# Kernel tuning notes

Measured on AMD Instinct MI355X. Metric: run time of the kernel, lower is better.

## Reference

```python
import jax, jax.numpy as jnp
import numpy as np


def setup_inputs() -> dict:
    key = jax.random.key(0)
    kq, kk, kv = jax.random.split(key, 3)
    B, T, D = 32, 2048, 64
    return {
        "queries": jax.random.normal(kq, (B, T, D), dtype=jnp.float32),
        "keys": jax.random.normal(kk, (B, T, D), dtype=jnp.float32),
        "values": jax.random.normal(kv, (B, T, D), dtype=jnp.float32),
    }


def reference(queries, keys, values):
    # scores: [B, T, T] = Q K^T / sqrt(d)
    d = queries.shape[-1]
    scale = 1.0 / jnp.sqrt(jnp.asarray(d, dtype=queries.dtype))
    scores = jnp.einsum("btd,bsd->bts", queries, keys) * scale
    T = scores.shape[-1]
    # causal lower-triangular mask; masked positions -> -inf before softmax
    causal = jnp.tril(jnp.ones((T, T), dtype=bool))
    scores = jnp.where(causal[None, :, :], scores, -jnp.inf)
    attn = jax.nn.softmax(scores, axis=-1)
    # eval mode: no dropout
    return jnp.einsum("bts,bsd->btd", attn, values)
```

## Files before the change

### kernel.cpp

```cpp
#include <hip/hip_runtime.h>
#include <hip/hip_bf16.h>

typedef __bf16 bf16;
typedef bf16 bf16x2 __attribute__((ext_vector_type(2)));
typedef bf16 bf16x8 __attribute__((ext_vector_type(8)));
typedef float f32x2 __attribute__((ext_vector_type(2)));
typedef float f32x4 __attribute__((ext_vector_type(4)));
typedef float f32x16 __attribute__((ext_vector_type(16)));
typedef unsigned int uint;

namespace {
constexpr int kB  = 32;
constexpr int kT  = 2048;
constexpr int kD  = 64;
constexpr int QB  = 128;
constexpr float THR = 8.f;
constexpr int CHUNK_F = 128 * 64 + 128 + 128;
constexpr size_t WS_NEED = (size_t)512 * CHUNK_F * 4;
}

__global__ __launch_bounds__(256, 2)
void fa_part(const float* __restrict__ Qg, const float* __restrict__ Kg,
             const float* __restrict__ Vg, float* __restrict__ Og,
             float* __restrict__ Wg, int mode) {
  const int tid  = (int)threadIdx.x;
  const int wid  = tid >> 6;
  const int lane = tid & 63;
  const int hi   = lane >> 5;
  const int ql   = lane & 31;

  const int bid = (int)blockIdx.x;
  const int b   = bid & 31;
  const int u   = bid >> 5;
  int j, t0, t1, sc = 0; bool split;
  if (mode) {
    static const signed char JT[24] = {15,15,7,14,14,13,13,6,12,12,11,11,5,10,10,9,9,4,8,8,3,2,1,0};
    static const signed char HT[24] = { 0, 1,-1, 0, 1, 0, 1,-1, 0, 1, 0, 1,-1, 0, 1, 0, 1,-1, 0, 1,-1,-1,-1,-1};
    j = JT[u]; const int h = HT[u];
    if (h < 0) { split = false; t0 = 0; t1 = 2 * (j + 1); }
    else { split = true; t0 = h * (j + 1); t1 = t0 + (j + 1); sc = b * 16 + 2 * (15 - j) + h; }
  } else {
    j = 15 - u; split = false; t0 = 0; t1 = 2 * (j + 1);
  }
  const int q0   = j * QB;
  const int qw   = q0 + wid * 32;
  const int qrow = qw + ql;

  __shared__ __align__(16) char smem[4 * 32 * 36 * 4];
  bf16* lK = (bf16*)smem;
  bf16* lV = (bf16*)(smem + 8192);

  const float* Qb = Qg + ((size_t)b * kT + qw) * kD;
  const float* Kb = Kg + (size_t)b * kT * kD;
  const float* Vb = Vg + (size_t)b * kT * kD;
  float*       Ob = Og + ((size_t)b * kT + qw) * kD;

  bf16x8 qf[4];
#pragma unroll
  for (int db = 0; db < 4; ++db) {
    const float* s = Qb + (size_t)ql * kD + db * 16 + hi * 8;
    f32x4 f0 = *(const f32x4*)s, f1 = *(const f32x4*)(s + 4);
    bf16x8 q;
#pragma unroll
    for (int jj = 0; jj < 4; ++jj) {
      q[jj]     = (bf16)(f0[jj] * 0.125f);
      q[jj + 4] = (bf16)(f1[jj] * 0.125f);
    }
    qf[db] = q;
  }

  f32x16 ot0 = {}, ot1 = {};
  float m_s = -1e30f, l_s = 0.f;

  const int krow = tid >> 2;
  const int kc16 = (tid & 3) << 4;
  const int vkey = (tid & 31) << 1;
  const int vd0  = (tid >> 5) << 3;

  f32x4 kp0, kp1, kp2, kp3, vp0, vp1, vp2, vp3;

#define LOADK(KV)                                                      \
  {                                                                    \
    const float* s_ = Kb + (size_t)((KV) + krow) * kD + kc16;          \
    kp0 = ((const f32x4*)s_)[0]; kp1 = ((const f32x4*)s_)[1];          \
    kp2 = ((const f32x4*)s_)[2]; kp3 = ((const f32x4*)s_)[3];          \
  }
#define LOADV(KV)                                                      \
  {                                                                    \
    const float* s0_ = Vb + (size_t)((KV) + vkey) * kD + vd0;          \
    const float* s1_ = s0_ + kD;                                       \
    vp0 = ((const f32x4*)s0_)[0]; vp1 = ((const f32x4*)s0_)[1];        \
    vp2 = ((const f32x4*)s1_)[0]; vp3 = ((const f32x4*)s1_)[1];        \
  }
#define STAGEK()                                                       \
  {                                                                    \
    bf16x8 h0_, h1_;                                                   \
    _Pragma("unroll") for (int jj = 0; jj < 4; ++jj) {                 \
      h0_[jj] = (bf16)kp0[jj]; h0_[jj + 4] = (bf16)kp1[jj];            \
      h1_[jj] = (bf16)kp2[jj]; h1_[jj + 4] = (bf16)kp3[jj];            \
    }                                                                  \
    *(bf16x8*)&lK[(krow * 64 + kc16)     ^ ((krow & 7) << 3)] = h0_;   \
    *(bf16x8*)&lK[(krow * 64 + kc16 + 8) ^ ((krow & 7) << 3)] = h1_;   \
  }
#define STAGEV()                                                       \
  {                                                                    \
    _Pragma("unroll") for (int jj = 0; jj < 8; ++jj) {                 \
      int d_ = vd0 + jj;                                               \
      float a0_ = (jj < 4) ? vp0[jj] : vp1[jj - 4];                    \
      float a1_ = (jj < 4) ? vp2[jj] : vp3[jj - 4];                    \
      int e_ = (d_ * 64 + vkey) ^ ((d_ & 7) << 3);                     \
      *(bf16x2*)&lV[e_] = (bf16x2){(bf16)a0_, (bf16)a1_};              \
    }                                                                  \
  }

  const int kv0 = t0 * 64, kv1 = t1 * 64;
  LOADK(kv0) LOADV(kv0)
  for (int kv = kv0; kv < kv1; kv += 64) {
    STAGEK() STAGEV()
    __syncthreads();
    if (kv + 64 < kv1) { LOADK(kv + 64) LOADV(kv + 64) }

    if (kv <= qw) {
      const int nkb = (kv + 32 <= qw) ? 2 : 1;

      f32x16 st0 = {}, st1 = {};
      __builtin_amdgcn_s_setprio(1);
#pragma unroll
      for (int db = 0; db < 4; ++db) {
        bf16x8 kf = *(const bf16x8*)&lK[(ql * 64 + db * 16 + hi * 8) ^ ((ql & 7) << 3)];
        st0 = __builtin_amdgcn_mfma_f32_32x32x16_bf16(kf, qf[db], st0, 0, 0, 0);
      }
      if (nkb == 2) {
        const int r1 = 32 + ql;
#pragma unroll
        for (int db = 0; db < 4; ++db) {
          bf16x8 kf = *(const bf16x8*)&lK[(r1 * 64 + db * 16 + hi * 8) ^ ((r1 & 7) << 3)];
          st1 = __builtin_amdgcn_mfma_f32_32x32x16_bf16(kf, qf[db], st1, 0, 0, 0);
        }
      }
      __builtin_amdgcn_s_setprio(0);

      if (kv + (nkb << 5) > qw) {
#pragma unroll
        for (int reg = 0; reg < 16; ++reg) {
          int krel = (reg & 3) + 8 * (reg >> 2) + 4 * hi;
          if (kv + krel > qrow) st0[reg] = -1e30f;
          if (nkb == 2 && kv + 32 + krel > qrow) st1[reg] = -1e30f;
        }
      }

      float mx = -1e30f;
#pragma unroll
      for (int r = 0; r < 16; ++r) mx = fmaxf(mx, st0[r]);
      if (nkb == 2) {
#pragma unroll
        for (int r = 0; r < 16; ++r) mx = fmaxf(mx, st1[r]);
      }
      mx = fmaxf(mx, __shfl_xor(mx, 32));
      const bool defer = (__all((mx - m_s) <= THR) != 0);
      float mn = m_s;
      if (!defer) {
        mn = fmaxf(m_s, mx);
        float corr = __expf(m_s - mn);
        m_s = mn;
        l_s *= corr;
#pragma unroll
        for (int r = 0; r < 16; ++r) { ot0[r] *= corr; ot1[r] *= corr; }
      }
      float ls = 0.f;
#pragma unroll
      for (int r = 0; r < 16; ++r) { float p = __expf(st0[r] - mn); st0[r] = p; ls += p; }
      if (nkb == 2) {
#pragma unroll
        for (int r = 0; r < 16; ++r) { float p = __expf(st1[r] - mn); st1[r] = p; ls += p; }
      }
      ls += __shfl_xor(ls, 32);
      l_s += ls;

      uint w_[16];
#pragma unroll
      for (int m = 0; m < 8; ++m) {
        bf16x2 t = {(bf16)st0[2 * m], (bf16)st0[2 * m + 1]};
        w_[m] = __builtin_bit_cast(uint, t);
      }
      if (nkb == 2) {
#pragma unroll
        for (int m = 0; m < 8; ++m) {
          bf16x2 t = {(bf16)st1[2 * m], (bf16)st1[2 * m + 1]};
          w_[8 + m] = __builtin_bit_cast(uint, t);
        }
      }

#pragma unroll
      for (int ks = 0; ks < 4; ++ks) {
        if (ks < 2 * nkb) {
          const int mb = (ks >> 1) * 8 + (ks & 1) * 4;
          uint a0 = w_[mb], a1 = w_[mb + 1], b0 = w_[mb + 2], b1 = w_[mb + 3];
          asm volatile("v_permlane32_swap_b32 %0, %1" : "+v"(a0), "+v"(b0));
          asm volatile("v_permlane32_swap_b32 %0, %1" : "+v"(a1), "+v"(b1));
          union { uint u4[4]; bf16x8 v; } pc;
          pc.u4[0] = a0; pc.u4[1] = a1; pc.u4[2] = b0; pc.u4[3] = b1;
          const bf16x8 pf = pc.v;
          __builtin_amdgcn_s_setprio(1);
          {
            bf16x8 vf0 = *(const bf16x8*)&lV[(ql * 64 + ks * 16 + hi * 8) ^ ((ql & 7) << 3)];
            ot0 = __builtin_amdgcn_mfma_f32_32x32x16_bf16(vf0, pf, ot0, 0, 0, 0);
            const int d1 = 32 + ql;
            bf16x8 vf1 = *(const bf16x8*)&lV[(d1 * 64 + ks * 16 + hi * 8) ^ ((d1 & 7) << 3)];
            ot1 = __builtin_amdgcn_mfma_f32_32x32x16_bf16(vf1, pf, ot1, 0, 0, 0);
          }
          __builtin_amdgcn_s_setprio(0);
        }
      }
    }
    __syncthreads();
  }

  const float scl = split ? 1.0f : (1.0f / l_s);
  float* outp = split ? (Wg + (size_t)sc * CHUNK_F + (size_t)(wid * 32) * kD) : Ob;
  float* ep = (float*)(void*)smem + wid * (32 * 36);
#pragma unroll
  for (int dt = 0; dt < 2; ++dt) {
    __syncthreads();
#pragma unroll
    for (int m = 0; m < 8; ++m) {
      int d = ((2 * m) & 3) + 8 * (m >> 1) + 4 * hi;
      f32x2 v;
      v[0] = (dt ? ot1[2 * m]     : ot0[2 * m])     * scl;
      v[1] = (dt ? ot1[2 * m + 1] : ot0[2 * m + 1]) * scl;
      *(f32x2*)&ep[ql * 36 + d] = v;
    }
    __syncthreads();
#pragma unroll
    for (int p = 0; p < 4; ++p) {
      int q = p * 8 + (lane >> 3);
      int cc = (lane & 7) * 4;
      f32x4 v = *(const f32x4*)&ep[q * 36 + cc];
      *(f32x4*)&outp[(size_t)q * kD + dt * 32 + cc] = v;
    }
  }
  if (split && hi == 0) {
    float* wm = Wg + (size_t)sc * CHUNK_F + 8192;
    wm[wid * 32 + ql]       = m_s;
    wm[128 + wid * 32 + ql] = l_s;
  }
}

__global__ __launch_bounds__(256)
void fa_merge(const float* __restrict__ Wg, float* __restrict__ Og) {
  const int bid = (int)blockIdx.x;
  const int b = bid >> 3, e = bid & 7;
  const int j = 8 + e;
  const float* w0 = Wg + (size_t)(b * 16 + 2 * (15 - j)) * CHUNK_F;
  const float* w1 = w0 + CHUNK_F;
  const int tid = (int)threadIdx.x;
  const int r = tid >> 1, ch = (tid & 1) * 32;
  const float m0 = w0[8192 + r], m1 = w1[8192 + r];
  const float l0 = w0[8320 + r], l1 = w1[8320 + r];
  const float M = fmaxf(m0, m1);
  float a = __expf(m0 - M), c = __expf(m1 - M);
  const float inv = 1.0f / (a * l0 + c * l1);
  a *= inv; c *= inv;
  float* orow = Og + ((size_t)b * kT + (size_t)j * QB + r) * kD + ch;
  const float* p0 = w0 + (size_t)r * kD + ch;
  const float* p1 = w1 + (size_t)r * kD + ch;
#pragma unroll
  for (int k = 0; k < 8; ++k) {
    f32x4 x0 = ((const f32x4*)p0)[k], x1 = ((const f32x4*)p1)[k];
    f32x4 o;
#pragma unroll
    for (int q = 0; q < 4; ++q) o[q] = a * x0[q] + c * x1[q];
    ((f32x4*)orow)[k] = o;
  }
}

extern "C" void kernel_launch(void* const* d_in, const int* in_sizes, int n_in,
                              void* d_out, int out_size, void* d_ws, size_t ws_size,
                              hipStream_t stream) {
  const float* Q = (const float*)d_in[0];
  const float* K = (const float*)d_in[1];
  const float* V = (const float*)d_in[2];
  float* O = (float*)d_out;
  const int mode = (ws_size >= WS_NEED) ? 1 : 0;
  dim3 grid(mode ? 24 * kB : 16 * kB);
  fa_part<<<grid, 256, 0, stream>>>(Q, K, V, O, (float*)d_ws, mode);
  if (mode) fa_merge<<<dim3(256), 256, 0, stream>>>((const float*)d_ws, O);
}
```

Measured before the change: 130.7 us.

## Split long causal query blocks into up to four KV partitions with merge kernel

Adds a finer split-KV mode in which query blocks 4-15 are divided into 2, 3 or 4 KV-range partitions according to their causal length. The grid grows from 24 to 40 blocks per batch, and a new merge kernel combines up to four partial outputs using their max and sum statistics. The aim is better load balance and more parallel work on the long causal rows, at the cost of more workspace traffic and merge work. This path only runs when the provided workspace is large enough.

```diff
diff --git a/kernel.cpp b/kernel.cpp
--- a/kernel.cpp
+++ b/kernel.cpp
@@ -16,7 +16,8 @@
 constexpr int QB  = 128;
 constexpr float THR = 8.f;
 constexpr int CHUNK_F = 128 * 64 + 128 + 128;
-constexpr size_t WS_NEED = (size_t)512 * CHUNK_F * 4;
+constexpr size_t WS1_NEED = (size_t)512  * CHUNK_F * 4;
+constexpr size_t WS2_NEED = (size_t)1152 * CHUNK_F * 4;
 }
 
 __global__ __launch_bounds__(256, 2)
@@ -33,7 +34,22 @@
   const int b   = bid & 31;
   const int u   = bid >> 5;
   int j, t0, t1, sc = 0; bool split;
-  if (mode) {
+  if (mode == 2) {
+    static const signed char JT2[40] = {15,15,15,15,14,14,14,14,13,13,13,13,12,12,12,12,
+                                        11,11,11,10,10,10,9,9,9,8,8,8,7,7,6,6,5,5,4,4,3,2,1,0};
+    static const signed char HT2[40] = {0,1,2,3,0,1,2,3,0,1,2,3,0,1,2,3,
+                                        0,1,2,0,1,2,0,1,2,0,1,2,0,1,0,1,0,1,0,1,0,0,0,0};
+    j = JT2[u]; const int h = HT2[u];
+    if (j < 4) { split = false; t0 = 0; t1 = 2 * (j + 1); }
+    else {
+      split = true;
+      const int T  = 2 * (j + 1);
+      const int nj = (j >= 12) ? 4 : ((j >= 8) ? 3 : 2);
+      t0 = (h * T) / nj; t1 = ((h + 1) * T) / nj;
+      const int off = (j < 8) ? ((j - 4) * 2) : ((j < 12) ? (8 + (j - 8) * 3) : (20 + (j - 12) * 4));
+      sc = b * 36 + off + h;
+    }
+  } else if (mode == 1) {
     static const signed char JT[24] = {15,15,7,14,14,13,13,6,12,12,11,11,5,10,10,9,9,4,8,8,3,2,1,0};
     static const signed char HT[24] = { 0, 1,-1, 0, 1, 0, 1,-1, 0, 1, 0, 1,-1, 0, 1, 0, 1,-1, 0, 1,-1,-1,-1,-1};
     j = JT[u]; const int h = HT[u];
@@ -274,6 +290,51 @@
   }
 }
 
+__global__ __launch_bounds__(256)
+void fa_merge2(const float* __restrict__ Wg, float* __restrict__ Og) {
+  const int bid = (int)blockIdx.x;
+  const int b = bid / 12, e = bid - b * 12;
+  const int j = 4 + e;
+  const int nj  = (j >= 12) ? 4 : ((j >= 8) ? 3 : 2);
+  const int off = (j < 8) ? ((j - 4) * 2) : ((j < 12) ? (8 + (j - 8) * 3) : (20 + (j - 12) * 4));
+  const float* base = Wg + (size_t)(b * 36 + off) * CHUNK_F;
+  const int tid = (int)threadIdx.x;
+  const int r = tid >> 1, ch = (tid & 1) * 32;
+  float m_[4], l_[4], a_[4];
+  float M = -1e30f;
+#pragma unroll
+  for (int i = 0; i < 4; ++i) {
+    if (i < nj) {
+      m_[i] = base[(size_t)i * CHUNK_F + 8192 + r];
+      l_[i] = base[(size_t)i * CHUNK_F + 8320 + r];
+      M = fmaxf(M, m_[i]);
+    } else { m_[i] = -1e30f; l_[i] = 0.f; }
+  }
+  float denom = 0.f;
+#pragma unroll
+  for (int i = 0; i < 4; ++i) {
+    a_[i] = (i < nj) ? __expf(m_[i] - M) : 0.f;
+    denom += a_[i] * l_[i];
+  }
+  const float inv = 1.0f / denom;
+#pragma unroll
+  for (int i = 0; i < 4; ++i) a_[i] *= inv;
+  float* orow = Og + ((size_t)b * kT + (size_t)j * QB + r) * kD + ch;
+#pragma unroll
+  for (int k = 0; k < 8; ++k) {
+    f32x4 o = {0.f, 0.f, 0.f, 0.f};
+#pragma unroll
+    for (int i = 0; i < 4; ++i) {
+      if (i < nj) {
+        f32x4 x = ((const f32x4*)(base + (size_t)i * CHUNK_F + (size_t)r * kD + ch))[k];
+#pragma unroll
+        for (int q = 0; q < 4; ++q) o[q] += a_[i] * x[q];
+      }
+    }
+    ((f32x4*)orow)[k] = o;
+  }
+}
+
 extern "C" void kernel_launch(void* const* d_in, const int* in_sizes, int n_in,
                               void* d_out, int out_size, void* d_ws, size_t ws_size,
                               hipStream_t stream) {
@@ -281,8 +342,9 @@
   const float* K = (const float*)d_in[1];
   const float* V = (const float*)d_in[2];
   float* O = (float*)d_out;
-  const int mode = (ws_size >= WS_NEED) ? 1 : 0;
-  dim3 grid(mode ? 24 * kB : 16 * kB);
+  const int mode = (ws_size >= WS2_NEED) ? 2 : (ws_size >= WS1_NEED) ? 1 : 0;
+  dim3 grid(mode == 2 ? 40 * kB : mode == 1 ? 24 * kB : 16 * kB);
   fa_part<<<grid, 256, 0, stream>>>(Q, K, V, O, (float*)d_ws, mode);
-  if (mode) fa_merge<<<dim3(256), 256, 0, stream>>>((const float*)d_ws, O);
-}
+  if (mode == 2)      fa_merge2<<<dim3(384), 256, 0, stream>>>((const float*)d_ws, O);
+  else if (mode == 1) fa_merge<<<dim3(256), 256, 0, stream>>>((const float*)d_ws, O);
+}
```

Result: slower. 155.2 us (+18.8%).
